# Performance work log

Measured on AMD Instinct MI355X. Metric: run time of the kernel, lower is better.

## Reference

```python
import jax, jax.numpy as jnp
import numpy as np

ALPHA = 0.1
MAX_ITER = 35
TOL = 0.01
STEP = ALPHA / 2.0  # step_size = alpha/2 as in TV2DFunction.forward


def _prox_tv1d(step, y):
    """Exact 1D TV prox via taut-string lower/upper hulls (faithful port of _prox_tv1d)."""
    n = y.shape[0]
    width = n + 1
    dt = y.dtype
    cs = jnp.cumsum(y)
    y_low = jnp.concatenate([jnp.zeros(1, dt), cs - step]).at[width - 1].add(step)
    y_up = jnp.concatenate([jnp.zeros(1, dt), cs + step]).at[width - 1].add(-step)

    inf = jnp.asarray(jnp.inf, dt)
    il = jnp.zeros(width, jnp.int32)   # index_low
    iu = jnp.zeros(width, jnp.int32)   # index_up
    idx = jnp.zeros(width, jnp.int32)  # breakpoint indices
    sl = jnp.zeros(width, dt).at[0].set(inf)    # slope_low
    su = jnp.zeros(width, dt).at[0].set(-inf)   # slope_up
    z = jnp.zeros(width, dt)
    zero = jnp.int32(0)

    def fdiv(num, a, b):
        # a > b always holds on the taken branch; maximum() only guards the
        # unselected jnp.where branch against NaN/Inf.
        return num / jnp.maximum(a - b, 1).astype(dt)

    def body(i, st):
        il, sl, iu, su, idx, z, s_l, c_l, s_u, c_u, c = st
        c_l = c_l + 1
        c_u = c_u + 1
        il = il.at[c_l].set(i)
        iu = iu.at[c_u].set(i)
        sl = sl.at[c_l].set(y_low[i] - y_low[i - 1])

        def w1_cond(t):
            il_, sl_, c_l_ = t
            return (c_l_ > s_l + 1) & (sl_[jnp.maximum(s_l, c_l_ - 1)] <= sl_[c_l_])

        def w1_body(t):
            il_, sl_, c_l_ = t
            c_l_ = c_l_ - 1
            il_ = il_.at[c_l_].set(i)
            ns = jnp.where(c_l_ > s_l + 1,
                           fdiv(y_low[i] - y_low[il_[c_l_ - 1]], i, il_[c_l_ - 1]),
                           fdiv(y_low[i] - z[c], i, idx[c]))
            return il_, sl_.at[c_l_].set(ns), c_l_

        il, sl, c_l = jax.lax.while_loop(w1_cond, w1_body, (il, sl, c_l))

        su = su.at[c_u].set(y_up[i] - y_up[i - 1])

        def w2_cond(t):
            iu_, su_, c_u_ = t
            return (c_u_ > s_u + 1) & (su_[jnp.maximum(s_u, c_u_ - 1)] >= su_[c_u_])

        def w2_body(t):
            iu_, su_, c_u_ = t
            c_u_ = c_u_ - 1
            iu_ = iu_.at[c_u_].set(i)
            ns = jnp.where(c_u_ > s_u + 1,
                           fdiv(y_up[i] - y_up[iu_[c_u_ - 1]], i, iu_[c_u_ - 1]),
                           fdiv(y_up[i] - z[c], i, idx[c]))
            return iu_, su_.at[c_u_].set(ns), c_u_

        iu, su, c_u = jax.lax.while_loop(w2_cond, w2_body, (iu, su, c_u))

        def w3_cond(t):
            idx_, z_, sl_, il_, s_u_, c_ = t
            return (c_l == s_l + 1) & (c_u > s_u_ + 1) & (sl_[c_l] >= su[s_u_ + 1])

        def w3_body(t):
            idx_, z_, sl_, il_, s_u_, c_ = t
            c_ = c_ + 1
            s_u_ = s_u_ + 1
            k = iu[s_u_]
            idx_ = idx_.at[c_].set(k)
            z_ = z_.at[c_].set(y_up[k])
            il_ = il_.at[s_l].set(k)
            sl_ = sl_.at[c_l].set(fdiv(y_low[i] - y_up[k], i, k))
            return idx_, z_, sl_, il_, s_u_, c_

        idx, z, sl, il, s_u, c = jax.lax.while_loop(w3_cond, w3_body, (idx, z, sl, il, s_u, c))

        def w4_cond(t):
            idx_, z_, su_, iu_, s_l_, c_ = t
            return (c_u == s_u + 1) & (c_l > s_l_ + 1) & (su_[c_u] <= sl[s_l_ + 1])

        def w4_body(t):
            idx_, z_, su_, iu_, s_l_, c_ = t
            c_ = c_ + 1
            s_l_ = s_l_ + 1
            k = il[s_l_]
            idx_ = idx_.at[c_].set(k)
            z_ = z_.at[c_].set(y_low[k])
            iu_ = iu_.at[s_u].set(k)
            su_ = su_.at[c_u].set(fdiv(y_up[i] - y_low[k], i, k))
            return idx_, z_, su_, iu_, s_l_, c_

        idx, z, su, iu, s_l, c = jax.lax.while_loop(w4_cond, w4_body, (idx, z, su, iu, s_l, c))

        return il, sl, iu, su, idx, z, s_l, c_l, s_u, c_u, c

    st = (il, sl, iu, su, idx, z, zero, zero, zero, zero, zero)
    il, sl, iu, su, idx, z, s_l, c_l, s_u, c_u, c = jax.lax.fori_loop(1, width, body, st)

    # tail: append remaining lower-hull points to the breakpoint list
    m = c_l - s_l
    offs = jnp.arange(width)
    valid = (offs >= 1) & (offs <= m)
    src = il[jnp.clip(s_l + offs, 0, width - 1)]
    tgt = jnp.where(valid, c + offs, width)  # 'width' is out of bounds -> dropped
    idx = idx.at[tgt].set(src, mode='drop')
    z = z.at[tgt].set(y_low[src], mode='drop')
    c = c + m

    # piecewise-constant output: slope of taut string on each segment
    a = (z - jnp.roll(z, 1)) / jnp.maximum(idx - jnp.roll(idx, 1), 1).astype(dt)
    knots = jnp.where(offs <= c, idx, n + 1)  # sorted; idx[c] == n
    seg = jnp.searchsorted(knots, jnp.arange(n), side='right')  # segment id in [1, c]
    return a[seg]


def _prox_cols(step, A):
    return jax.vmap(lambda col: _prox_tv1d(step, col), in_axes=1, out_axes=1)(A)


def _prox_rows(step, A):
    return jax.vmap(lambda row: _prox_tv1d(step, row))(A)


def _prox_tv2d(x, step, max_iter, tol):
    """Douglas-Rachford splitting for 2D TV prox (Barbero & Sra 2014)."""
    def cond(carry):
        it, x_, p, q, acc = carry
        return (it < max_iter) & (acc >= tol)

    def body(carry):
        it, x_, p, q, _ = carry
        y = _prox_cols(step, x_ + p)
        p = p + x_ - y
        x2 = _prox_rows(step, y + q)
        q = q + y - x2
        acc = jnp.max(jnp.abs(y - x2))
        return it + 1, x2, p, q, acc

    z0 = jnp.zeros_like(x)
    init = (jnp.int32(0), x, z0, z0, jnp.asarray(jnp.inf, x.dtype))
    return jax.lax.while_loop(cond, body, init)[1]


def setup_inputs() -> dict:
    key = jax.random.key(0)
    X = jax.random.normal(key, (256, 256), dtype=jnp.float32)
    return {"X": X}


def reference(X):
    return _prox_tv2d(X, STEP, MAX_ITER, TOL)
```

## Files before the change

### kernel.cpp

```cpp
#include <hip/hip_runtime.h>

#define N 256
#define NB 256
#define NT 64
#define LAM 0.05f
#define TWOLAM (2.0f * LAM)
#define FOURLAM (4.0f * LAM)
#define MAXIT 35
#define TOL 0.01f
#define SLOTSTRIDE 2
#define POLLBUDGET (1 << 17)

typedef unsigned long long u64;

__device__ __forceinline__ float rlane(float v, int lane) {
    return __int_as_float(__builtin_amdgcn_readlane(__float_as_int(v), lane));
}

__device__ __forceinline__ void gstore(float* p, float v) {
    __hip_atomic_store(p, v, __ATOMIC_RELAXED, __HIP_MEMORY_SCOPE_AGENT);
}
__device__ __forceinline__ u64 ald(const u64* p) {
    return __hip_atomic_load(p, __ATOMIC_RELAXED, __HIP_MEMORY_SCOPE_AGENT);
}
__device__ __forceinline__ void ast(u64* p, u64 v) {
    __hip_atomic_store(p, v, __ATOMIC_RELAXED, __HIP_MEMORY_SCOPE_AGENT);
}

__device__ __forceinline__ void gload_col(const float* mat, int c, int lane, float& a,
                                          float& b, float& d, float& e) {
    const float* p0 = mat + (size_t)lane * N + c;
    const float* p1 = p0 + 64 * N;
    const float* p2 = p0 + 128 * N;
    const float* p3 = p0 + 192 * N;
    asm volatile("global_load_dword %0, %4, off sc0 sc1\n\t"
                 "global_load_dword %1, %5, off sc0 sc1\n\t"
                 "global_load_dword %2, %6, off sc0 sc1\n\t"
                 "global_load_dword %3, %7, off sc0 sc1\n\t"
                 "s_waitcnt vmcnt(0)"
                 : "=&v"(a), "=&v"(b), "=&v"(d), "=&v"(e)
                 : "v"(p0), "v"(p1), "v"(p2), "v"(p3)
                 : "memory");
}

struct Dist { float r0, r1, r2, r3; };

__device__ __forceinline__ float dfetch(const Dist& d, int k) {
    const int lane = k & 63;
    const int sel = k >> 6;
    float a = rlane(d.r0, lane);
    float b = rlane(d.r1, lane);
    float c = rlane(d.r2, lane);
    float e = rlane(d.r3, lane);
    float ab = (sel & 1) ? b : a;
    float ce = (sel & 1) ? e : c;
    return (sel & 2) ? ce : ab;
}

__device__ __forceinline__ void flushseg(Dist& o, int lo, int hi, float val, int lane) {
    const unsigned len = (unsigned)(hi - lo);
    const int base = lane - lo;
    o.r0 = ((unsigned)(base      ) <= len) ? val : o.r0;
    o.r1 = ((unsigned)(base + 64 ) <= len) ? val : o.r1;
    o.r2 = ((unsigned)(base + 128) <= len) ? val : o.r2;
    o.r3 = ((unsigned)(base + 192) <= len) ? val : o.r3;
}

__device__ __forceinline__ u64 sel4(u64 a, u64 b, u64 c, u64 d, int r) {
    u64 ab = (r & 1) ? b : a;
    u64 cd = (r & 1) ? d : c;
    return (r & 2) ? cd : ab;
}

__device__ __forceinline__ unsigned wredmax(unsigned x) {
    unsigned t;
    t = (unsigned)__builtin_amdgcn_update_dpp(0, (int)x, 0x111, 0xf, 0xf, true); x = x > t ? x : t;
    t = (unsigned)__builtin_amdgcn_update_dpp(0, (int)x, 0x112, 0xf, 0xf, true); x = x > t ? x : t;
    t = (unsigned)__builtin_amdgcn_update_dpp(0, (int)x, 0x114, 0xf, 0xf, true); x = x > t ? x : t;
    t = (unsigned)__builtin_amdgcn_update_dpp(0, (int)x, 0x118, 0xf, 0xf, true); x = x > t ? x : t;
    t = (unsigned)__builtin_amdgcn_update_dpp(0, (int)x, 0x142, 0xf, 0xf, true); x = x > t ? x : t;
    t = (unsigned)__builtin_amdgcn_update_dpp(0, (int)x, 0x143, 0xf, 0xf, true); x = x > t ? x : t;
    return (unsigned)__builtin_amdgcn_readlane((int)x, 63);
}


__device__ __forceinline__ void pollcol(const u64* m, int c, unsigned seq, int lane, Dist& v) {
    const u64* p0 = m + (size_t)lane * N + c;
    const u64* p1 = p0 + 64 * N;
    const u64* p2 = p0 + 128 * N;
    const u64* p3 = p0 + 192 * N;
    u64 f0 = ald(p0), f1 = ald(p1), f2 = ald(p2), f3 = ald(p3);
    int spin = 0;
    for (;;) {
        u64 g0 = ald(p0), g1 = ald(p1), g2 = ald(p2), g3 = ald(p3);
        const bool ok = ((unsigned)f0 >= seq) & ((unsigned)f1 >= seq) &
                        ((unsigned)f2 >= seq) & ((unsigned)f3 >= seq);
        if (__all((int)ok)) break;
        if (__builtin_expect(++spin > POLLBUDGET, 0)) break;
        f0 = g0; f1 = g1; f2 = g2; f3 = g3;
    }
    v.r0 = __uint_as_float((unsigned)(f0 >> 32));
    v.r1 = __uint_as_float((unsigned)(f1 >> 32));
    v.r2 = __uint_as_float((unsigned)(f2 >> 32));
    v.r3 = __uint_as_float((unsigned)(f3 >> 32));
}

__device__ __forceinline__ void storerow(u64* m, int row, unsigned seq, const Dist& o, int lane) {
    u64* r = m + (size_t)row * N;
    ast(r + lane,       ((u64)__float_as_uint(o.r0) << 32) | (u64)seq);
    ast(r + lane + 64,  ((u64)__float_as_uint(o.r1) << 32) | (u64)seq);
    ast(r + lane + 128, ((u64)__float_as_uint(o.r2) << 32) | (u64)seq);
    ast(r + lane + 192, ((u64)__float_as_uint(o.r3) << 32) | (u64)seq);
}

__device__ void tv1d_scan(const Dist& v, Dist& o, const int lane)
{
    const float lam = LAM, mlam = -LAM, twolam = TWOLAM;

    Dist vnx;
    {
        float a0 = __shfl_down(v.r0, 1), a1 = __shfl_down(v.r1, 1);
        float a2 = __shfl_down(v.r2, 1), a3 = __shfl_down(v.r3, 1);
        const bool hi = (lane == 63);
        vnx.r0 = hi ? rlane(v.r1, 0) : a0;
        vnx.r1 = hi ? rlane(v.r2, 0) : a1;
        vnx.r2 = hi ? rlane(v.r3, 0) : a2;
        vnx.r3 = hi ? v.r3 : a3;
    }
    Dist d;
    d.r0 = vnx.r0 - v.r0;  d.r1 = vnx.r1 - v.r1;
    d.r2 = vnx.r2 - v.r2;  d.r3 = vnx.r3 - v.r3;
    const unsigned lambits = __float_as_uint(lam);
    Dist sl;
    sl.r0 = __uint_as_float((__float_as_uint(d.r0) & 0x80000000u) | lambits);
    sl.r1 = __uint_as_float((__float_as_uint(d.r1) & 0x80000000u) | lambits);
    sl.r2 = __uint_as_float((__float_as_uint(d.r2) & 0x80000000u) | lambits);
    sl.r3 = __uint_as_float((__float_as_uint(d.r3) & 0x80000000u) | lambits);
    Dist slp;
    {
        float b0 = __shfl_up(sl.r0, 1), b1 = __shfl_up(sl.r1, 1);
        float b2 = __shfl_up(sl.r2, 1), b3 = __shfl_up(sl.r3, 1);
        const bool lo = (lane == 0);
        slp.r0 = lo ? 0.0f : b0;
        slp.r1 = lo ? rlane(sl.r0, 63) : b1;
        slp.r2 = lo ? rlane(sl.r1, 63) : b2;
        slp.r3 = lo ? rlane(sl.r2, 63) : b3;
    }
    Dist e, g;
    {
        float t0 = v.r0 - slp.r0, t1 = v.r1 - slp.r1, t2 = v.r2 - slp.r2, t3 = v.r3 - slp.r3;
        e.r0 = t0 + sl.r0;  e.r1 = t1 + sl.r1;  e.r2 = t2 + sl.r2;  e.r3 = t3 + sl.r3;
        g.r0 = t0 - lam;    g.r1 = t1 - lam;    g.r2 = t2 - lam;    g.r3 = t3 - lam;
    }
    const u64 S0 = __ballot(d.r0 < 0.0f);
    const u64 S1 = __ballot(d.r1 < 0.0f);
    const u64 S2 = __ballot(d.r2 < 0.0f);
    const u64 S3 = __ballot(d.r3 < 0.0f);
    const u64 B20 = __ballot(fabsf(d.r0) > TWOLAM);
    const u64 B21 = __ballot(fabsf(d.r1) > TWOLAM);
    const u64 B22 = __ballot(fabsf(d.r2) > TWOLAM);
    const u64 B23 = __ballot(fabsf(d.r3) > TWOLAM);
    const u64 B40 = __ballot(fabsf(d.r0) > FOURLAM);
    const u64 B41 = __ballot(fabsf(d.r1) > FOURLAM);
    const u64 B42 = __ballot(fabsf(d.r2) > FOURLAM);
    const u64 B43 = __ballot(fabsf(d.r3) > FOURLAM);
    const u64 Sp0 = (S0 << 1);
    const u64 Sp1 = (S1 << 1) | (S0 >> 63);
    const u64 Sp2 = (S2 << 1) | (S1 >> 63);
    const u64 Sp3 = (S3 << 1) | (S2 >> 63);
    const u64 NF0 = ~(B40 | (B20 & ~(S0 ^ Sp0)));
    const u64 NF1 = ~(B41 | (B21 & ~(S1 ^ Sp1)));
    const u64 NF2 = ~(B42 | (B22 & ~(S2 ^ Sp2)));
    const u64 NF3 = ~((B43 | (B23 & ~(S3 ^ Sp3))) & 0x7FFFFFFFFFFFFFFFull);
    const u64 FNn0 = (S0 & B20) | (~S0 & B40);
    const u64 FNn1 = (S1 & B21) | (~S1 & B41);
    const u64 FNn2 = (S2 & B22) | (~S2 & B42);
    const u64 FNn3 = (S3 & B23) | (~S3 & B43);
    const u64 FNp0 = (~S0 & B20) | (S0 & B40);
    const u64 FNp1 = (~S1 & B21) | (S1 & B41);
    const u64 FNp2 = (~S2 & B22) | (S2 & B42);
    const u64 FNp3 = (~S3 & B23) | (S3 & B43);
    const int initFF = (int)(B40 & 1ull);

    auto firstnf = [&](int jmin) -> int {
        const int w = jmin >> 6;
        u64 m = sel4(NF0, NF1, NF2, NF3, w) >> (jmin & 63);
        if (m) return jmin + (int)__builtin_ctzll(m);
        u64 m1 = (w < 1) ? NF1 : 0ull;
        u64 m2 = (w < 2) ? NF2 : 0ull;
        if (m1) return 64 + (int)__builtin_ctzll(m1);
        if (m2) return 128 + (int)__builtin_ctzll(m2);
        return 192 + (int)__builtin_ctzll(NF3);
    };

    auto trigbit = [&](int kk, int neg) -> int {
        const int w = kk >> 6;
        const u64 m = neg ? sel4(FNn0, FNn1, FNn2, FNn3, w)
                          : sel4(FNp0, FNp1, FNp2, FNp3, w);
        return (int)((m >> (kk & 63)) & 1ull);
    };

    int k = 0, k0 = 0, km = 0, kp = 0;
    float umin = lam, umax = mlam;
    const float v0 = rlane(v.r0, 0);
    float vmin = v0 - lam, vmax = v0 + lam;
    float flen = 1.0f;
    float rnext = 0.5f;
    float vn1 = rlane(vnx.r0, 0);

    auto fastfwd = [&]() {
        const int K1 = firstnf(k + 1);
        const int sneg = (int)((sel4(S0, S1, S2, S3, k >> 6) >> (k & 63)) & 1ull);
        flushseg(o, k, k, sneg ? vmin : vmax, lane);
        if (K1 > k + 1) {
            const int lo = k + 1;
            const unsigned len = (unsigned)(K1 - 1 - lo);
            const int base = lane - lo;
            o.r0 = ((unsigned)(base      ) <= len) ? e.r0 : o.r0;
            o.r1 = ((unsigned)(base + 64 ) <= len) ? e.r1 : o.r1;
            o.r2 = ((unsigned)(base + 128) <= len) ? e.r2 : o.r2;
            o.r3 = ((unsigned)(base + 192) <= len) ? e.r3 : o.r3;
        }
        k = K1; k0 = K1; km = K1; kp = K1;
        vmin = dfetch(g, K1);
        vmax = vmin + twolam;
        umin = lam; umax = mlam;
        flen = 1.0f; rnext = 0.5f;
        vn1 = dfetch(vnx, K1);
    };

    auto do_step = [&]() {
        const float un = umin + vn1 - vmin;
        const float ux = umax + vn1 - vmax;
        const bool neg = un < mlam;
        const bool pos = ux > lam;
        const int wn = (k + 1) >> 6, bn = (k + 1) & 63;
        const int tn = (int)((sel4(FNn0, FNn1, FNn2, FNn3, wn) >> bn) & 1ull);
        const int tp = (int)((sel4(FNp0, FNp1, FNp2, FNp3, wn) >> bn) & 1ull);
        if (__builtin_expect((int)(neg | pos), 1)) {
            const float fval = neg ? vmin : vmax;
            const int   fhi  = neg ? km : kp;
            flushseg(o, k0, fhi, fval, lane);
            const int k0n = fhi + 1;
            float vstar;
            int trig;
            if (__builtin_expect((int)(k0n <= k), 0)) {
                vstar = dfetch(v, k0n);
                trig = trigbit(k0n, (int)neg);
            } else {
                vstar = vn1;
                trig = neg ? tn : tp;
            }
            k = k0n; k0 = k0n; km = k0n; kp = k0n;
            vmin = neg ? vstar : vstar - twolam;
            vmax = vmin + twolam;
            umin = lam; umax = mlam;
            flen = 1.0f; rnext = 0.5f;
            if (k < N - 1 && trig) {
                fastfwd();
            } else {
                vn1 = dfetch(vnx, k);
            }
        } else {
            k++;
            const float r = rnext;
            flen += 1.0f;
            const bool cmin = (un >= lam);
            const bool cmax = (ux <= mlam);
            vmin = cmin ? fmaf(un - lam, r, vmin) : vmin;
            km   = cmin ? k : km;
            umin = cmin ? lam : un;
            vmax = cmax ? fmaf(ux + lam, r, vmax) : vmax;
            kp   = cmax ? k : kp;
            umax = cmax ? mlam : ux;
            vn1 = dfetch(vnx, k);
            rnext = __builtin_amdgcn_rcpf(flen + 1.0f);
        }
    };

    if (initFF) fastfwd();

    for (;;) {
        while (k < N - 1) {
            do_step();
            if (k >= N - 1) break;
            do_step();
        }
        for (;;) {
            if (umin < 0.0f) {
                flushseg(o, k0, km, vmin, lane);
                k0 = km + 1;
                if (k0 > N - 1) return;
                km = k = k0;
                vmin = dfetch(v, k0);
                umin = lam;
                umax = vmin + lam - vmax;
                flen = 1.0f;
            } else if (umax > 0.0f) {
                flushseg(o, k0, kp, vmax, lane);
                k0 = kp + 1;
                if (k0 > N - 1) return;
                kp = k = k0;
                vmax = dfetch(v, k0);
                umax = mlam;
                umin = vmax - lam - vmin;
                flen = 1.0f;
            } else {
                vmin += umin / flen;
                flushseg(o, k0, k, vmin, lane);
                return;
            }
            if (k != N - 1) break;
        }
        rnext = 0.5f;
        vn1 = dfetch(vnx, k);
    }
}

__global__ __launch_bounds__(NT) void tv2d_fused(const float* __restrict__ X,
                                                 float* __restrict__ out,
                                                 u64* __restrict__ ytg,
                                                 u64* __restrict__ xwg,
                                                 u64* __restrict__ accs)
{
    const int lane = threadIdx.x;
    const int b = blockIdx.x;

    Dist p = {0.f, 0.f, 0.f, 0.f};
    Dist q = {0.f, 0.f, 0.f, 0.f};
    Dist xout = {0.f, 0.f, 0.f, 0.f};

    for (int it = 0; it < MAXIT; ++it) {
        Dist v, o;
        if (it == 0) {
            gload_col(X, b, lane, v.r0, v.r1, v.r2, v.r3);
        } else {
            pollcol(xwg + (size_t)((it - 1) & 1) * (N * N), b, (unsigned)it, lane, v);
        }
        v.r0 += p.r0;  v.r1 += p.r1;  v.r2 += p.r2;  v.r3 += p.r3;

        const u64* ab = accs + (size_t)((it - 1) & 1) * (N * 2);
        const u64 *qa0 = ab + (size_t)lane * 2,        *qa1 = ab + (size_t)(lane + 64) * 2,
                  *qa2 = ab + (size_t)(lane + 128) * 2, *qa3 = ab + (size_t)(lane + 192) * 2;
        u64 a0 = 0, a1 = 0, a2 = 0, a3 = 0;
        if (it >= 1) {
            asm volatile("global_load_dwordx2 %0, %4, off sc0 sc1\n\t"
                         "global_load_dwordx2 %1, %5, off sc0 sc1\n\t"
                         "global_load_dwordx2 %2, %6, off sc0 sc1\n\t"
                         "global_load_dwordx2 %3, %7, off sc0 sc1"
                         : "=&v"(a0), "=&v"(a1), "=&v"(a2), "=&v"(a3)
                         : "v"(qa0), "v"(qa1), "v"(qa2), "v"(qa3)
                         : "memory");
        }

        tv1d_scan(v, o, lane);
        p.r0 = v.r0 - o.r0;  p.r1 = v.r1 - o.r1;
        p.r2 = v.r2 - o.r2;  p.r3 = v.r3 - o.r3;

        if (it >= 1) {
            asm volatile("s_waitcnt vmcnt(0)" ::: "memory");
            const unsigned seq = (unsigned)it;
            int spin = 0;
            for (;;) {
                const bool ok = ((unsigned)a0 >= seq) & ((unsigned)a1 >= seq) &
                                ((unsigned)a2 >= seq) & ((unsigned)a3 >= seq);
                if (__all((int)ok)) break;
                if (__builtin_expect(++spin > POLLBUDGET, 0)) break;
                a0 = ald(qa0); a1 = ald(qa1); a2 = ald(qa2); a3 = ald(qa3);
            }
            unsigned ma = (unsigned)(a0 >> 32), mb = (unsigned)(a1 >> 32);
            unsigned mc = (unsigned)(a2 >> 32), md = (unsigned)(a3 >> 32);
            ma = ma > mb ? ma : mb;  mc = mc > md ? mc : md;  ma = ma > mc ? ma : mc;
            const unsigned gm = wredmax(ma);
            if (__uint_as_float(gm) < TOL) break;
        }

        storerow(ytg + (size_t)(it & 1) * (N * N), b, (unsigned)(it + 1), o, lane);

        Dist yv, w, o2;
        pollcol(ytg + (size_t)(it & 1) * (N * N), b, (unsigned)(it + 1), lane, yv);
        w.r0 = yv.r0 + q.r0;
        w.r1 = yv.r1 + q.r1;
        w.r2 = yv.r2 + q.r2;
        w.r3 = yv.r3 + q.r3;
        tv1d_scan(w, o2, lane);
        q.r0 = w.r0 - o2.r0;  q.r1 = w.r1 - o2.r1;
        q.r2 = w.r2 - o2.r2;  q.r3 = w.r3 - o2.r3;
        xout = o2;

        float am = fmaxf(fmaxf(fabsf(yv.r0 - o2.r0), fabsf(yv.r1 - o2.r1)),
                         fmaxf(fabsf(yv.r2 - o2.r2), fabsf(yv.r3 - o2.r3)));
        const unsigned amu = wredmax(__float_as_uint(am));

        if (it < MAXIT - 1) {
            storerow(xwg + (size_t)(it & 1) * (N * N), b, (unsigned)(it + 1), o2, lane);
            if (lane == 0)
                ast((u64*)(accs + (size_t)(it & 1) * (N * 2)) + (size_t)b * 2,
                    ((u64)amu << 32) | (u64)(unsigned)(it + 1));
        }
    }

    float* xr = out + (size_t)b * N;
    xr[lane]       = xout.r0;
    xr[lane + 64]  = xout.r1;
    xr[lane + 128] = xout.r2;
    xr[lane + 192] = xout.r3;
}

template <bool WANT>
__device__ __forceinline__ unsigned wavebar(u64* slots, unsigned seq,
                                            unsigned payload, int line, int lane)
{
    __builtin_amdgcn_s_waitcnt(0);
    __hip_atomic_store(&slots[line * SLOTSTRIDE],
                       ((u64)payload << 32) | (u64)seq,
                       __ATOMIC_RELAXED, __HIP_MEMORY_SCOPE_AGENT);
    auto ld = [&](int i) {
        return __hip_atomic_load(&slots[i * SLOTSTRIDE],
                                 __ATOMIC_RELAXED, __HIP_MEMORY_SCOPE_AGENT);
    };
    u64 f0 = ld(lane), f1 = ld(lane + 64), f2 = ld(lane + 128), f3 = ld(lane + 192);
    for (;;) {
        u64 g0 = ld(lane), g1 = ld(lane + 64), g2 = ld(lane + 128), g3 = ld(lane + 192);
        const bool ok = ((unsigned)f0 >= seq) & ((unsigned)f1 >= seq) &
                        ((unsigned)f2 >= seq) & ((unsigned)f3 >= seq);
        if (__all((int)ok)) break;
        f0 = g0; f1 = g1; f2 = g2; f3 = g3;
    }
    unsigned ga = 0u;
    if (WANT) {
        unsigned a = (unsigned)(f0 >> 32), b = (unsigned)(f1 >> 32);
        unsigned c = (unsigned)(f2 >> 32), d = (unsigned)(f3 >> 32);
        a = a > b ? a : b;  c = c > d ? c : d;  a = a > c ? a : c;
        ga = wredmax(a);
    }
    return ga;
}

__global__ __launch_bounds__(NT) void tv2d_coop(const float* __restrict__ X,
                                                float* __restrict__ xw,
                                                float* __restrict__ yt,
                                                u64* __restrict__ slots)
{
    const int lane = threadIdx.x;
    const int b = blockIdx.x;

    Dist p = {0.f, 0.f, 0.f, 0.f};
    Dist q = {0.f, 0.f, 0.f, 0.f};
    unsigned accprev = 0u;

    for (int it = 0; it < MAXIT; ++it) {
        const float* xs = (it == 0) ? X : xw;
        Dist v, o;
        gload_col(xs, b, lane, v.r0, v.r1, v.r2, v.r3);
        v.r0 += p.r0;  v.r1 += p.r1;  v.r2 += p.r2;  v.r3 += p.r3;
        tv1d_scan(v, o, lane);
        p.r0 = v.r0 - o.r0;  p.r1 = v.r1 - o.r1;
        p.r2 = v.r2 - o.r2;  p.r3 = v.r3 - o.r3;
        float* yr = yt + b * N;
        gstore(yr + lane,       o.r0);
        gstore(yr + lane + 64,  o.r1);
        gstore(yr + lane + 128, o.r2);
        gstore(yr + lane + 192, o.r3);
        wavebar<false>(slots, 2u * (unsigned)it + 1u, accprev, b, lane);

        Dist yv, w, o2;
        gload_col(yt, b, lane, yv.r0, yv.r1, yv.r2, yv.r3);
        w.r0 = yv.r0 + q.r0;
        w.r1 = yv.r1 + q.r1;
        w.r2 = yv.r2 + q.r2;
        w.r3 = yv.r3 + q.r3;
        tv1d_scan(w, o2, lane);
        float d0 = yv.r0 - o2.r0;
        float d1 = yv.r1 - o2.r1;
        float d2 = yv.r2 - o2.r2;
        float d3 = yv.r3 - o2.r3;
        q.r0 = w.r0 - o2.r0;  q.r1 = w.r1 - o2.r1;
        q.r2 = w.r2 - o2.r2;  q.r3 = w.r3 - o2.r3;
        float* xr = xw + b * N;
        gstore(xr + lane,       o2.r0);
        gstore(xr + lane + 64,  o2.r1);
        gstore(xr + lane + 128, o2.r2);
        gstore(xr + lane + 192, o2.r3);

        float am = fmaxf(fmaxf(fabsf(d0), fabsf(d1)), fmaxf(fabsf(d2), fabsf(d3)));
        const unsigned amu = wredmax(__float_as_uint(am));

        if (it == MAXIT - 1) break;

        const unsigned ga = wavebar<true>(slots, 2u * (unsigned)it + 2u, amu, b, lane);
        if (__uint_as_float(ga) < TOL) break;
        accprev = amu;
    }
}

extern "C" void kernel_launch(void* const* d_in, const int* in_sizes, int n_in,
                              void* d_out, int out_size, void* d_ws, size_t ws_size,
                              hipStream_t stream) {
    const float* X = (const float*)d_in[0];
    float* xw = (float*)d_out;

    const size_t need = (size_t)4 * N * N * sizeof(u64)
                      + (size_t)2 * N * 2 * sizeof(u64);
    if (ws_size >= need) {
        u64* ytg  = (u64*)d_ws;
        u64* xwg  = ytg + (size_t)2 * N * N;
        u64* accs = xwg + (size_t)2 * N * N;
        (void)hipMemsetAsync(d_ws, 0, need, stream);
        void* args[] = { (void*)&X, (void*)&xw, (void*)&ytg, (void*)&xwg, (void*)&accs };
        (void)hipLaunchCooperativeKernel((void*)tv2d_fused, dim3(NB), dim3(NT), args, 0, stream);
    } else {
        float* yt = (float*)d_ws;
        u64* slots = (u64*)((char*)d_ws + (size_t)N * N * sizeof(float));
        (void)hipMemsetAsync((void*)slots, 0, N * SLOTSTRIDE * sizeof(u64), stream);
        void* args[] = { (void*)&X, (void*)&xw, (void*)&yt, (void*)&slots };
        (void)hipLaunchCooperativeKernel((void*)tv2d_coop, dim3(NB), dim3(NT), args, 0, stream);
    }
}
```

Measured before the change: 288.4 us.

## Replace fully flag-tagged fused kernel with half-tagged variant using a global barrier

The default path switches from a kernel where both the column and row exchanges use per-element sequence-tagged data with double buffering to one where only the column-to-row exchange (ytg) carries per-element flags. The row results are written as plain floats and synchronised with a grid-wide wave barrier that also reduces the convergence metric. This removes the tagged-xw polling and the separate accumulator loads, but puts a full barrier back on each iteration's critical path. It also adds a spin budget to the barrier loop.

```diff
diff --git a/kernel.cpp b/kernel.cpp
--- a/kernel.cpp
+++ b/kernel.cpp
@@ -82,7 +82,6 @@
     t = (unsigned)__builtin_amdgcn_update_dpp(0, (int)x, 0x143, 0xf, 0xf, true); x = x > t ? x : t;
     return (unsigned)__builtin_amdgcn_readlane((int)x, 63);
 }
-
 
 __device__ __forceinline__ void pollcol(const u64* m, int c, unsigned seq, int lane, Dist& v) {
     const u64* p0 = m + (size_t)lane * N + c;
@@ -317,96 +316,6 @@
     }
 }
 
-__global__ __launch_bounds__(NT) void tv2d_fused(const float* __restrict__ X,
-                                                 float* __restrict__ out,
-                                                 u64* __restrict__ ytg,
-                                                 u64* __restrict__ xwg,
-                                                 u64* __restrict__ accs)
-{
-    const int lane = threadIdx.x;
-    const int b = blockIdx.x;
-
-    Dist p = {0.f, 0.f, 0.f, 0.f};
-    Dist q = {0.f, 0.f, 0.f, 0.f};
-    Dist xout = {0.f, 0.f, 0.f, 0.f};
-
-    for (int it = 0; it < MAXIT; ++it) {
-        Dist v, o;
-        if (it == 0) {
-            gload_col(X, b, lane, v.r0, v.r1, v.r2, v.r3);
-        } else {
-            pollcol(xwg + (size_t)((it - 1) & 1) * (N * N), b, (unsigned)it, lane, v);
-        }
-        v.r0 += p.r0;  v.r1 += p.r1;  v.r2 += p.r2;  v.r3 += p.r3;
-
-        const u64* ab = accs + (size_t)((it - 1) & 1) * (N * 2);
-        const u64 *qa0 = ab + (size_t)lane * 2,        *qa1 = ab + (size_t)(lane + 64) * 2,
-                  *qa2 = ab + (size_t)(lane + 128) * 2, *qa3 = ab + (size_t)(lane + 192) * 2;
-        u64 a0 = 0, a1 = 0, a2 = 0, a3 = 0;
-        if (it >= 1) {
-            asm volatile("global_load_dwordx2 %0, %4, off sc0 sc1\n\t"
-                         "global_load_dwordx2 %1, %5, off sc0 sc1\n\t"
-                         "global_load_dwordx2 %2, %6, off sc0 sc1\n\t"
-                         "global_load_dwordx2 %3, %7, off sc0 sc1"
-                         : "=&v"(a0), "=&v"(a1), "=&v"(a2), "=&v"(a3)
-                         : "v"(qa0), "v"(qa1), "v"(qa2), "v"(qa3)
-                         : "memory");
-        }
-
-        tv1d_scan(v, o, lane);
-        p.r0 = v.r0 - o.r0;  p.r1 = v.r1 - o.r1;
-        p.r2 = v.r2 - o.r2;  p.r3 = v.r3 - o.r3;
-
-        if (it >= 1) {
-            asm volatile("s_waitcnt vmcnt(0)" ::: "memory");
-            const unsigned seq = (unsigned)it;
-            int spin = 0;
-            for (;;) {
-                const bool ok = ((unsigned)a0 >= seq) & ((unsigned)a1 >= seq) &
-                                ((unsigned)a2 >= seq) & ((unsigned)a3 >= seq);
-                if (__all((int)ok)) break;
-                if (__builtin_expect(++spin > POLLBUDGET, 0)) break;
-                a0 = ald(qa0); a1 = ald(qa1); a2 = ald(qa2); a3 = ald(qa3);
-            }
-            unsigned ma = (unsigned)(a0 >> 32), mb = (unsigned)(a1 >> 32);
-            unsigned mc = (unsigned)(a2 >> 32), md = (unsigned)(a3 >> 32);
-            ma = ma > mb ? ma : mb;  mc = mc > md ? mc : md;  ma = ma > mc ? ma : mc;
-            const unsigned gm = wredmax(ma);
-            if (__uint_as_float(gm) < TOL) break;
-        }
-
-        storerow(ytg + (size_t)(it & 1) * (N * N), b, (unsigned)(it + 1), o, lane);
-
-        Dist yv, w, o2;
-        pollcol(ytg + (size_t)(it & 1) * (N * N), b, (unsigned)(it + 1), lane, yv);
-        w.r0 = yv.r0 + q.r0;
-        w.r1 = yv.r1 + q.r1;
-        w.r2 = yv.r2 + q.r2;
-        w.r3 = yv.r3 + q.r3;
-        tv1d_scan(w, o2, lane);
-        q.r0 = w.r0 - o2.r0;  q.r1 = w.r1 - o2.r1;
-        q.r2 = w.r2 - o2.r2;  q.r3 = w.r3 - o2.r3;
-        xout = o2;
-
-        float am = fmaxf(fmaxf(fabsf(yv.r0 - o2.r0), fabsf(yv.r1 - o2.r1)),
-                         fmaxf(fabsf(yv.r2 - o2.r2), fabsf(yv.r3 - o2.r3)));
-        const unsigned amu = wredmax(__float_as_uint(am));
-
-        if (it < MAXIT - 1) {
-            storerow(xwg + (size_t)(it & 1) * (N * N), b, (unsigned)(it + 1), o2, lane);
-            if (lane == 0)
-                ast((u64*)(accs + (size_t)(it & 1) * (N * 2)) + (size_t)b * 2,
-                    ((u64)amu << 32) | (u64)(unsigned)(it + 1));
-        }
-    }
-
-    float* xr = out + (size_t)b * N;
-    xr[lane]       = xout.r0;
-    xr[lane + 64]  = xout.r1;
-    xr[lane + 128] = xout.r2;
-    xr[lane + 192] = xout.r3;
-}
-
 template <bool WANT>
 __device__ __forceinline__ unsigned wavebar(u64* slots, unsigned seq,
                                             unsigned payload, int line, int lane)
@@ -420,11 +329,13 @@
                                  __ATOMIC_RELAXED, __HIP_MEMORY_SCOPE_AGENT);
     };
     u64 f0 = ld(lane), f1 = ld(lane + 64), f2 = ld(lane + 128), f3 = ld(lane + 192);
+    int spin = 0;
     for (;;) {
         u64 g0 = ld(lane), g1 = ld(lane + 64), g2 = ld(lane + 128), g3 = ld(lane + 192);
         const bool ok = ((unsigned)f0 >= seq) & ((unsigned)f1 >= seq) &
                         ((unsigned)f2 >= seq) & ((unsigned)f3 >= seq);
         if (__all((int)ok)) break;
+        if (__builtin_expect(++spin > POLLBUDGET, 0)) break;
         f0 = g0; f1 = g1; f2 = g2; f3 = g3;
     }
     unsigned ga = 0u;
@@ -435,6 +346,53 @@
         ga = wredmax(a);
     }
     return ga;
+}
+
+__global__ __launch_bounds__(NT) void tv2d_half(const float* __restrict__ X,
+                                                float* __restrict__ xw,
+                                                u64* __restrict__ ytg,
+                                                u64* __restrict__ slots)
+{
+    const int lane = threadIdx.x;
+    const int b = blockIdx.x;
+
+    Dist p = {0.f, 0.f, 0.f, 0.f};
+    Dist q = {0.f, 0.f, 0.f, 0.f};
+
+    for (int it = 0; it < MAXIT; ++it) {
+        const float* xs = (it == 0) ? X : xw;
+        Dist v, o;
+        gload_col(xs, b, lane, v.r0, v.r1, v.r2, v.r3);
+        v.r0 += p.r0;  v.r1 += p.r1;  v.r2 += p.r2;  v.r3 += p.r3;
+        tv1d_scan(v, o, lane);
+        p.r0 = v.r0 - o.r0;  p.r1 = v.r1 - o.r1;
+        p.r2 = v.r2 - o.r2;  p.r3 = v.r3 - o.r3;
+        storerow(ytg, b, (unsigned)(it + 1), o, lane);
+
+        Dist yv, w, o2;
+        pollcol(ytg, b, (unsigned)(it + 1), lane, yv);
+        w.r0 = yv.r0 + q.r0;
+        w.r1 = yv.r1 + q.r1;
+        w.r2 = yv.r2 + q.r2;
+        w.r3 = yv.r3 + q.r3;
+        tv1d_scan(w, o2, lane);
+        q.r0 = w.r0 - o2.r0;  q.r1 = w.r1 - o2.r1;
+        q.r2 = w.r2 - o2.r2;  q.r3 = w.r3 - o2.r3;
+        float* xr = xw + (size_t)b * N;
+        gstore(xr + lane,       o2.r0);
+        gstore(xr + lane + 64,  o2.r1);
+        gstore(xr + lane + 128, o2.r2);
+        gstore(xr + lane + 192, o2.r3);
+
+        float am = fmaxf(fmaxf(fabsf(yv.r0 - o2.r0), fabsf(yv.r1 - o2.r1)),
+                         fmaxf(fabsf(yv.r2 - o2.r2), fabsf(yv.r3 - o2.r3)));
+        const unsigned amu = wredmax(__float_as_uint(am));
+
+        if (it == MAXIT - 1) break;
+
+        const unsigned ga = wavebar<true>(slots, (unsigned)(it + 1), amu, b, lane);
+        if (__uint_as_float(ga) < TOL) break;
+    }
 }
 
 __global__ __launch_bounds__(NT) void tv2d_coop(const float* __restrict__ X,
@@ -500,15 +458,14 @@
     const float* X = (const float*)d_in[0];
     float* xw = (float*)d_out;
 
-    const size_t need = (size_t)4 * N * N * sizeof(u64)
-                      + (size_t)2 * N * 2 * sizeof(u64);
+    const size_t need = (size_t)N * N * sizeof(u64)
+                      + (size_t)N * SLOTSTRIDE * sizeof(u64);
     if (ws_size >= need) {
-        u64* ytg  = (u64*)d_ws;
-        u64* xwg  = ytg + (size_t)2 * N * N;
-        u64* accs = xwg + (size_t)2 * N * N;
+        u64* ytg   = (u64*)d_ws;
+        u64* slots = ytg + (size_t)N * N;
         (void)hipMemsetAsync(d_ws, 0, need, stream);
-        void* args[] = { (void*)&X, (void*)&xw, (void*)&ytg, (void*)&xwg, (void*)&accs };
-        (void)hipLaunchCooperativeKernel((void*)tv2d_fused, dim3(NB), dim3(NT), args, 0, stream);
+        void* args[] = { (void*)&X, (void*)&xw, (void*)&ytg, (void*)&slots };
+        (void)hipLaunchCooperativeKernel((void*)tv2d_half, dim3(NB), dim3(NT), args, 0, stream);
     } else {
         float* yt = (float*)d_ws;
         u64* slots = (u64*)((char*)d_ws + (size_t)N * N * sizeof(float));
```

Result: faster. 272.0 us (-5.7%).

## Single-buffer tagged exchange arrays and merge convergence poll into row poll

Applied to the files above, without the earlier changes.

Drops double buffering of the sequence-tagged y and x exchange matrices, so each is written in place with monotone sequence tags, halving workspace and memset size. The convergence-flag poll is merged into the column poll of the y matrix, so one spin loop waits for both the data and the previous iteration's residuals. The fallback kernel replaces its first wave barrier with tagged y stores and polls, and the poll budget is reduced. Single buffering relies on the ordering of tagged stores to avoid a fast block overwriting data that a slow block has not yet read. The smaller budget raises the chance of timing out early and using stale data.

```diff
diff --git a/kernel.cpp b/kernel.cpp
--- a/kernel.cpp
+++ b/kernel.cpp
@@ -9,7 +9,7 @@
 #define MAXIT 35
 #define TOL 0.01f
 #define SLOTSTRIDE 2
-#define POLLBUDGET (1 << 17)
+#define POLLBUDGET (1 << 15)
 
 typedef unsigned long long u64;
 
@@ -83,7 +83,6 @@
     return (unsigned)__builtin_amdgcn_readlane((int)x, 63);
 }
 
-
 __device__ __forceinline__ void pollcol(const u64* m, int c, unsigned seq, int lane, Dist& v) {
     const u64* p0 = m + (size_t)lane * N + c;
     const u64* p1 = p0 + 64 * N;
@@ -103,6 +102,41 @@
     v.r1 = __uint_as_float((unsigned)(f1 >> 32));
     v.r2 = __uint_as_float((unsigned)(f2 >> 32));
     v.r3 = __uint_as_float((unsigned)(f3 >> 32));
+}
+
+__device__ __forceinline__ unsigned pollrow(const u64* ytg, const u64* ab, int b,
+                                            unsigned seqy, unsigned seqa, int lane, Dist& v) {
+    const u64* p0 = ytg + (size_t)lane * N + b;
+    const u64* p1 = p0 + 64 * N;
+    const u64* p2 = p0 + 128 * N;
+    const u64* p3 = p0 + 192 * N;
+    const u64* q0 = ab + (size_t)lane * 2;
+    const u64* q1 = ab + (size_t)(lane + 64) * 2;
+    const u64* q2 = ab + (size_t)(lane + 128) * 2;
+    const u64* q3 = ab + (size_t)(lane + 192) * 2;
+    u64 f0 = ald(p0), f1 = ald(p1), f2 = ald(p2), f3 = ald(p3);
+    u64 a0 = ald(q0), a1 = ald(q1), a2 = ald(q2), a3 = ald(q3);
+    int spin = 0;
+    for (;;) {
+        u64 g0 = ald(p0), g1 = ald(p1), g2 = ald(p2), g3 = ald(p3);
+        u64 h0 = ald(q0), h1 = ald(q1), h2 = ald(q2), h3 = ald(q3);
+        const bool ok = ((unsigned)f0 >= seqy) & ((unsigned)f1 >= seqy) &
+                        ((unsigned)f2 >= seqy) & ((unsigned)f3 >= seqy) &
+                        ((unsigned)a0 >= seqa) & ((unsigned)a1 >= seqa) &
+                        ((unsigned)a2 >= seqa) & ((unsigned)a3 >= seqa);
+        if (__all((int)ok)) break;
+        if (__builtin_expect(++spin > POLLBUDGET, 0)) break;
+        f0 = g0; f1 = g1; f2 = g2; f3 = g3;
+        a0 = h0; a1 = h1; a2 = h2; a3 = h3;
+    }
+    v.r0 = __uint_as_float((unsigned)(f0 >> 32));
+    v.r1 = __uint_as_float((unsigned)(f1 >> 32));
+    v.r2 = __uint_as_float((unsigned)(f2 >> 32));
+    v.r3 = __uint_as_float((unsigned)(f3 >> 32));
+    unsigned ma = (unsigned)(a0 >> 32), mb = (unsigned)(a1 >> 32);
+    unsigned mc = (unsigned)(a2 >> 32), md = (unsigned)(a3 >> 32);
+    ma = ma > mb ? ma : mb;  mc = mc > md ? mc : md;  ma = ma > mc ? ma : mc;
+    return wredmax(ma);
 }
 
 __device__ __forceinline__ void storerow(u64* m, int row, unsigned seq, const Dist& o, int lane) {
@@ -317,11 +351,11 @@
     }
 }
 
-__global__ __launch_bounds__(NT) void tv2d_fused(const float* __restrict__ X,
-                                                 float* __restrict__ out,
-                                                 u64* __restrict__ ytg,
-                                                 u64* __restrict__ xwg,
-                                                 u64* __restrict__ accs)
+__global__ __launch_bounds__(NT) void tv2d_lean(const float* __restrict__ X,
+                                                float* __restrict__ out,
+                                                u64* __restrict__ ytg,
+                                                u64* __restrict__ xwg,
+                                                u64* __restrict__ accs)
 {
     const int lane = threadIdx.x;
     const int b = blockIdx.x;
@@ -335,50 +369,21 @@
         if (it == 0) {
             gload_col(X, b, lane, v.r0, v.r1, v.r2, v.r3);
         } else {
-            pollcol(xwg + (size_t)((it - 1) & 1) * (N * N), b, (unsigned)it, lane, v);
+            pollcol(xwg, b, (unsigned)it, lane, v);
         }
         v.r0 += p.r0;  v.r1 += p.r1;  v.r2 += p.r2;  v.r3 += p.r3;
-
-        const u64* ab = accs + (size_t)((it - 1) & 1) * (N * 2);
-        const u64 *qa0 = ab + (size_t)lane * 2,        *qa1 = ab + (size_t)(lane + 64) * 2,
-                  *qa2 = ab + (size_t)(lane + 128) * 2, *qa3 = ab + (size_t)(lane + 192) * 2;
-        u64 a0 = 0, a1 = 0, a2 = 0, a3 = 0;
-        if (it >= 1) {
-            asm volatile("global_load_dwordx2 %0, %4, off sc0 sc1\n\t"
-                         "global_load_dwordx2 %1, %5, off sc0 sc1\n\t"
-                         "global_load_dwordx2 %2, %6, off sc0 sc1\n\t"
-                         "global_load_dwordx2 %3, %7, off sc0 sc1"
-                         : "=&v"(a0), "=&v"(a1), "=&v"(a2), "=&v"(a3)
-                         : "v"(qa0), "v"(qa1), "v"(qa2), "v"(qa3)
-                         : "memory");
-        }
-
         tv1d_scan(v, o, lane);
         p.r0 = v.r0 - o.r0;  p.r1 = v.r1 - o.r1;
         p.r2 = v.r2 - o.r2;  p.r3 = v.r3 - o.r3;
-
-        if (it >= 1) {
-            asm volatile("s_waitcnt vmcnt(0)" ::: "memory");
-            const unsigned seq = (unsigned)it;
-            int spin = 0;
-            for (;;) {
-                const bool ok = ((unsigned)a0 >= seq) & ((unsigned)a1 >= seq) &
-                                ((unsigned)a2 >= seq) & ((unsigned)a3 >= seq);
-                if (__all((int)ok)) break;
-                if (__builtin_expect(++spin > POLLBUDGET, 0)) break;
-                a0 = ald(qa0); a1 = ald(qa1); a2 = ald(qa2); a3 = ald(qa3);
-            }
-            unsigned ma = (unsigned)(a0 >> 32), mb = (unsigned)(a1 >> 32);
-            unsigned mc = (unsigned)(a2 >> 32), md = (unsigned)(a3 >> 32);
-            ma = ma > mb ? ma : mb;  mc = mc > md ? mc : md;  ma = ma > mc ? ma : mc;
-            const unsigned gm = wredmax(ma);
-            if (__uint_as_float(gm) < TOL) break;
-        }
-
-        storerow(ytg + (size_t)(it & 1) * (N * N), b, (unsigned)(it + 1), o, lane);
-
-        Dist yv, w, o2;
-        pollcol(ytg + (size_t)(it & 1) * (N * N), b, (unsigned)(it + 1), lane, yv);
+        storerow(ytg, b, (unsigned)(it + 1), o, lane);
+
+        Dist yv;
+        const u64* ab = accs + (size_t)((it - 1) & 1) * (N * 2);
+        const unsigned gm = pollrow(ytg, ab, b, (unsigned)(it + 1),
+                                    (it >= 1) ? (unsigned)it : 0u, lane, yv);
+        if (it >= 1 && __uint_as_float(gm) < TOL) break;
+
+        Dist w, o2;
         w.r0 = yv.r0 + q.r0;
         w.r1 = yv.r1 + q.r1;
         w.r2 = yv.r2 + q.r2;
@@ -393,7 +398,7 @@
         const unsigned amu = wredmax(__float_as_uint(am));
 
         if (it < MAXIT - 1) {
-            storerow(xwg + (size_t)(it & 1) * (N * N), b, (unsigned)(it + 1), o2, lane);
+            storerow(xwg, b, (unsigned)(it + 1), o2, lane);
             if (lane == 0)
                 ast((u64*)(accs + (size_t)(it & 1) * (N * 2)) + (size_t)b * 2,
                     ((u64)amu << 32) | (u64)(unsigned)(it + 1));
@@ -420,11 +425,13 @@
                                  __ATOMIC_RELAXED, __HIP_MEMORY_SCOPE_AGENT);
     };
     u64 f0 = ld(lane), f1 = ld(lane + 64), f2 = ld(lane + 128), f3 = ld(lane + 192);
+    int spin = 0;
     for (;;) {
         u64 g0 = ld(lane), g1 = ld(lane + 64), g2 = ld(lane + 128), g3 = ld(lane + 192);
         const bool ok = ((unsigned)f0 >= seq) & ((unsigned)f1 >= seq) &
                         ((unsigned)f2 >= seq) & ((unsigned)f3 >= seq);
         if (__all((int)ok)) break;
+        if (__builtin_expect(++spin > POLLBUDGET, 0)) break;
         f0 = g0; f1 = g1; f2 = g2; f3 = g3;
     }
     unsigned ga = 0u;
@@ -437,9 +444,9 @@
     return ga;
 }
 
-__global__ __launch_bounds__(NT) void tv2d_coop(const float* __restrict__ X,
+__global__ __launch_bounds__(NT) void tv2d_half(const float* __restrict__ X,
                                                 float* __restrict__ xw,
-                                                float* __restrict__ yt,
+                                                u64* __restrict__ ytg,
                                                 u64* __restrict__ slots)
 {
     const int lane = threadIdx.x;
@@ -447,7 +454,6 @@
 
     Dist p = {0.f, 0.f, 0.f, 0.f};
     Dist q = {0.f, 0.f, 0.f, 0.f};
-    unsigned accprev = 0u;
 
     for (int it = 0; it < MAXIT; ++it) {
         const float* xs = (it == 0) ? X : xw;
@@ -457,40 +463,31 @@
         tv1d_scan(v, o, lane);
         p.r0 = v.r0 - o.r0;  p.r1 = v.r1 - o.r1;
         p.r2 = v.r2 - o.r2;  p.r3 = v.r3 - o.r3;
-        float* yr = yt + b * N;
-        gstore(yr + lane,       o.r0);
-        gstore(yr + lane + 64,  o.r1);
-        gstore(yr + lane + 128, o.r2);
-        gstore(yr + lane + 192, o.r3);
-        wavebar<false>(slots, 2u * (unsigned)it + 1u, accprev, b, lane);
+        storerow(ytg, b, (unsigned)(it + 1), o, lane);
 
         Dist yv, w, o2;
-        gload_col(yt, b, lane, yv.r0, yv.r1, yv.r2, yv.r3);
+        pollcol(ytg, b, (unsigned)(it + 1), lane, yv);
         w.r0 = yv.r0 + q.r0;
         w.r1 = yv.r1 + q.r1;
         w.r2 = yv.r2 + q.r2;
         w.r3 = yv.r3 + q.r3;
         tv1d_scan(w, o2, lane);
-        float d0 = yv.r0 - o2.r0;
-        float d1 = yv.r1 - o2.r1;
-        float d2 = yv.r2 - o2.r2;
-        float d3 = yv.r3 - o2.r3;
         q.r0 = w.r0 - o2.r0;  q.r1 = w.r1 - o2.r1;
         q.r2 = w.r2 - o2.r2;  q.r3 = w.r3 - o2.r3;
-        float* xr = xw + b * N;
+        float* xr = xw + (size_t)b * N;
         gstore(xr + lane,       o2.r0);
         gstore(xr + lane + 64,  o2.r1);
         gstore(xr + lane + 128, o2.r2);
         gstore(xr + lane + 192, o2.r3);
 
-        float am = fmaxf(fmaxf(fabsf(d0), fabsf(d1)), fmaxf(fabsf(d2), fabsf(d3)));
+        float am = fmaxf(fmaxf(fabsf(yv.r0 - o2.r0), fabsf(yv.r1 - o2.r1)),
+                         fmaxf(fabsf(yv.r2 - o2.r2), fabsf(yv.r3 - o2.r3)));
         const unsigned amu = wredmax(__float_as_uint(am));
 
         if (it == MAXIT - 1) break;
 
-        const unsigned ga = wavebar<true>(slots, 2u * (unsigned)it + 2u, amu, b, lane);
+        const unsigned ga = wavebar<true>(slots, (unsigned)(it + 1), amu, b, lane);
         if (__uint_as_float(ga) < TOL) break;
-        accprev = amu;
     }
 }
 
@@ -500,20 +497,21 @@
     const float* X = (const float*)d_in[0];
     float* xw = (float*)d_out;
 
-    const size_t need = (size_t)4 * N * N * sizeof(u64)
+    const size_t need = (size_t)2 * N * N * sizeof(u64)
                       + (size_t)2 * N * 2 * sizeof(u64);
     if (ws_size >= need) {
         u64* ytg  = (u64*)d_ws;
-        u64* xwg  = ytg + (size_t)2 * N * N;
-        u64* accs = xwg + (size_t)2 * N * N;
+        u64* xwg  = ytg + (size_t)N * N;
+        u64* accs = xwg + (size_t)N * N;
         (void)hipMemsetAsync(d_ws, 0, need, stream);
         void* args[] = { (void*)&X, (void*)&xw, (void*)&ytg, (void*)&xwg, (void*)&accs };
-        (void)hipLaunchCooperativeKernel((void*)tv2d_fused, dim3(NB), dim3(NT), args, 0, stream);
+        (void)hipLaunchCooperativeKernel((void*)tv2d_lean, dim3(NB), dim3(NT), args, 0, stream);
     } else {
-        float* yt = (float*)d_ws;
-        u64* slots = (u64*)((char*)d_ws + (size_t)N * N * sizeof(float));
-        (void)hipMemsetAsync((void*)slots, 0, N * SLOTSTRIDE * sizeof(u64), stream);
-        void* args[] = { (void*)&X, (void*)&xw, (void*)&yt, (void*)&slots };
-        (void)hipLaunchCooperativeKernel((void*)tv2d_coop, dim3(NB), dim3(NT), args, 0, stream);
-    }
-}
+        u64* ytg   = (u64*)d_ws;
+        u64* slots = ytg + (size_t)N * N;
+        (void)hipMemsetAsync(d_ws, 0, (size_t)N * N * sizeof(u64)
+                                     + (size_t)N * SLOTSTRIDE * sizeof(u64), stream);
+        void* args[] = { (void*)&X, (void*)&xw, (void*)&ytg, (void*)&slots };
+        (void)hipLaunchCooperativeKernel((void*)tv2d_half, dim3(NB), dim3(NT), args, 0, stream);
+    }
+}
```

New measurement: 291.4 us. About the same (+1.1%).
